# Kernel tuning notes

Measured on AMD Instinct MI355X. Metric: run time of the kernel, lower is better.

## Reference

```python
import jax, jax.numpy as jnp
import numpy as np

F_FILT = 40      # num_filters
K_GABOR = 401    # n_coefficients
K_POOL = 401     # window_length
HOP = 160        # hop_length
SR = 16000
EPS_PCEN = 1e-6
EPS_IN = 1e-5    # nn.InstanceNorm1d default eps
B, T = 8, 160000


def _hz2mel(f):
    return 2595.0 * np.log10(1.0 + f / 700.0)


def _mel2hz(m):
    return 700.0 * (10.0 ** (m / 2595.0) - 1.0)


def setup_inputs() -> dict:
    key = jax.random.key(0)
    x = jax.random.normal(key, (B, 1, T), dtype=jnp.float32)
    # mel-spaced Gabor center frequencies / bandwidths (filter_init_method='mel')
    edges = _mel2hz(np.linspace(_hz2mel(60.0), _hz2mel(7800.0), F_FILT + 2))
    center = edges[1:-1]
    fwhm = np.maximum(edges[2:] - edges[:-2], 1.0)
    eta = 2.0 * np.pi * center / SR                      # rad/sample
    sigma = np.sqrt(2.0 * np.log(2.0)) / (np.pi * fwhm / SR)  # samples
    ones = jnp.ones(F_FILT, jnp.float32)
    return {
        "x": x,
        "gabor_eta": jnp.asarray(eta, jnp.float32),
        "gabor_sigma": jnp.asarray(sigma, jnp.float32),
        "pool_bandwidths": 0.4 * ones,   # GaussianLowPass init
        "pool_bias": ones,               # GaussianLowPass bias init (ones)
        "ema_weights": 0.04 * ones,      # sPCEN smoothing_coefficient, per-channel
        "alpha": 0.96 * ones,
        "delta": 2.0 * ones,
        "root": 0.96 * ones,             # root=compression_factor=0.96
    }


def _conv1d(x, w, stride=1, groups=1):
    # x: (N, C, T), w: (O, C//groups, K); cross-correlation like torch F.conv1d
    return jax.lax.conv_general_dilated(
        x, w, (stride,), "VALID",
        dimension_numbers=("NCH", "OIH", "NCH"),
        feature_group_count=groups)


def _ema_scan(x, s):
    # y_0 = x_0 ; y_t = s*x_t + (1-s)*y_{t-1}  (per-channel s), parallel scan
    s3 = s[None, :, None]
    a = jnp.broadcast_to(1.0 - s3, x.shape)
    b = s3 * x
    a = a.at[:, :, 0].set(0.0)
    b = b.at[:, :, 0].set(x[:, :, 0])
    def comb(c1, c2):
        a1, b1 = c1
        a2, b2 = c2
        return a1 * a2, a2 * b1 + b2
    _, y = jax.lax.associative_scan(comb, (a, b), axis=2)
    return y


def reference(x, gabor_eta, gabor_sigma, pool_bandwidths, pool_bias,
              ema_weights, alpha, delta, root):
    dt = x.dtype
    # --- Gabor complex conv frontend -> |.|^2 ---
    t = jnp.arange(K_GABOR, dtype=dt) - (K_GABOR - 1) / 2.0
    env = jnp.exp(-0.5 * (t[None] / gabor_sigma[:, None]) ** 2) \
          / (jnp.sqrt(2.0 * jnp.pi) * gabor_sigma[:, None])
    phase = gabor_eta[:, None] * t[None]
    kern = jnp.stack([env * jnp.cos(phase), env * jnp.sin(phase)], axis=1)
    kern = kern.reshape(2 * F_FILT, 1, K_GABOR)
    xp = jnp.pad(x, ((0, 0), (0, 0), (K_GABOR - 1, 0)))  # causal pad
    y = _conv1d(xp, kern)                                 # (B, 2F, T)
    y = y.reshape(y.shape[0], F_FILT, 2, y.shape[-1])
    power = y[:, :, 0] ** 2 + y[:, :, 1] ** 2             # |z|^2, (B, F, T)

    # --- sPCEN compression ---
    s = jnp.clip(ema_weights, 0.0, 1.0)
    ema = _ema_scan(power, s)
    a3 = jnp.minimum(alpha, 1.0)[None, :, None]
    inv_r = (1.0 / jnp.maximum(root, 1.0))[None, :, None]
    d3 = delta[None, :, None]
    comp = (power / (EPS_PCEN + ema) ** a3 + d3) ** inv_r - d3 ** inv_r

    # --- Gaussian low-pass depthwise pooling (causal, stride=HOP) ---
    bw = jnp.clip(pool_bandwidths, 2.0 / K_POOL, 0.5)
    tp = jnp.arange(-K_POOL // 2, K_POOL // 2, dtype=dt)  # -201..199, len 401
    den = bw * 0.5 * (K_POOL - 1)
    pk = jnp.exp(-0.5 * (tp[None] / den[:, None]) ** 2).reshape(F_FILT, 1, K_POOL)
    cp = jnp.pad(comp, ((0, 0), (0, 0), (K_POOL - 1, 0)))
    pooled = _conv1d(cp, pk, stride=HOP, groups=F_FILT) + pool_bias[None, :, None]

    # --- InstanceNorm1d (affine=False, biased var, eps=1e-5) ---
    m = pooled.mean(-1, keepdims=True)
    v = pooled.var(-1, keepdims=True)
    return (pooled - m) / jnp.sqrt(v + EPS_IN)
```

## Files before the change

kernel.cpp:

```cpp
#include <hip/hip_runtime.h>
#include <math.h>

#define F_FILT   40
#define K_GABOR  401
#define HOP      160
#define T_LEN    160000
#define B_BATCH  8
#define EPS_PCENF 1e-6f
#define EPS_INF   1e-5f

#define NG       5
#define GF       8
#define NKMAX    13
#define TC       640
#define UW       10
#define NCH1     250
#define OPOFF    544
#define XPAIRS   (OPOFF + 544)
#define NSTG     136

#define THREADS  320
#define NWAVES   5
#define RT       10
#define TILE     3200
#define TPC      10
#define CHUNKS   5
#define NPT      20
#define NPOOL_BLK 200
#define KP       208
#define HALOP    200
#define TILEP    1600
#define RINGP    1800

typedef _Float16 h2_t  __attribute__((ext_vector_type(2)));
typedef _Float16 half8 __attribute__((ext_vector_type(8)));
typedef float    f32x4 __attribute__((ext_vector_type(4)));

__device__ __forceinline__ float fdot2(h2_t a, h2_t b, float c) {
    return __builtin_amdgcn_fdot2(a, b, c, false);
}
__device__ __forceinline__ unsigned pk2(float a, float b) {
    return __builtin_bit_cast(unsigned, __builtin_amdgcn_cvt_pkrtz(a, b));
}
__device__ __forceinline__ h2_t bch(unsigned u) {
    return __builtin_bit_cast(h2_t, u);
}
__device__ __forceinline__ float fexp2(float x) { return __builtin_amdgcn_exp2f(x); }
__device__ __forceinline__ float flog2(float x) { return __builtin_amdgcn_logf(x); }

__device__ __forceinline__ void group_span(float sigma0, int& klo, int& nk) {
    const int R = min(200, (int)ceilf(4.5f * sigma0));
    klo = (200 - R) & ~31;
    nk  = ((200 + R - klo) >> 5) + 1;
    if (nk > NKMAX) nk = NKMAX;
}

__global__ __launch_bounds__(256) void leaf_weights(
    const float* __restrict__ eta_g, const float* __restrict__ sigma_g,
    const float* __restrict__ bw_g,
    _Float16* __restrict__ Atab, unsigned* __restrict__ pktab)
{
    const int gi = blockIdx.x;
    const int f0 = gi * GF;
    int klo, nk;
    group_span(sigma_g[f0], klo, nk);

    for (int idx = threadIdx.x; idx < 52 * 16 * 8; idx += 256) {
        const int c8 = idx >> 7;
        const int m  = (idx >> 3) & 15;
        const int i  = idx & 7;
        const int f  = f0 + (m >> 1);
        const int k  = klo + c8 * 8 + i;
        float w = 0.f;
        if (k <= 400) {
            const float sg = sigma_g[f];
            const float t  = (float)(k - 200);
            const float z  = t / sg;
            const float e  = (0.3989422804014327f / sg) * expf(-0.5f * z * z);
            const float ph = eta_g[f] * t;
            w = (m & 1) ? e * sinf(ph) : e * cosf(ph);
        }
        Atab[(size_t)(gi * 52 + c8) * 128 + m * 8 + i] = (_Float16)w;
    }
    for (int idx = threadIdx.x; idx < GF * KP; idx += 256) {
        const int fl = idx / KP, i = idx % KP;
        const int f = f0 + fl;
        const float bw  = fminf(fmaxf(bw_g[f], 2.0f / 401.0f), 0.5f);
        const float den = bw * 0.5f * 400.0f;
        float pp[2];
        for (int j = 0; j < 2; ++j) {
            int k = 2 * i + j;
            float pv = 0.f;
            if (k < K_GABOR) {
                float tp = (float)(k - 201);
                float d = tp / den;
                pv = expf(-0.5f * d * d);
            }
            pp[j] = pv;
        }
        pktab[f * KP + i] = pk2(pp[0], pp[1]);
    }
}

__device__ __forceinline__ uint4 ld4(const unsigned* __restrict__ xp, int p) {
    uint4 v; v.x = xp[p]; v.y = xp[p + 1]; v.z = xp[p + 2]; v.w = xp[p + 3];
    return v;
}

template<int NK>
__device__ __forceinline__ void conv_kloop(
    const unsigned* __restrict__ xpair, const uint4* __restrict__ Ap,
    int aBase, int pB, f32x4* acc)
{
    uint4 F[UW];
#pragma unroll
    for (int u = 0; u < UW; ++u) F[u] = ld4(xpair, pB + 8 * u);
#pragma unroll
    for (int jk = 0; jk < NK; ++jk) {
        const half8 aCur = __builtin_bit_cast(half8, Ap[aBase + jk * 64]);
#pragma unroll
        for (int u = 0; u < UW; ++u) {
            acc[u] = __builtin_amdgcn_mfma_f32_16x16x32_f16(
                aCur, __builtin_bit_cast(half8, F[u]), acc[u], 0, 0, 0);
        }
        if (jk + 1 < NK) {
#pragma unroll
            for (int u = 0; u < UW - 2; ++u) F[u] = F[u + 2];
            F[UW - 2] = ld4(xpair, pB + 16 * (jk + 1) + 8 * (UW - 2));
            F[UW - 1] = ld4(xpair, pB + 16 * (jk + 1) + 8 * (UW - 1));
        }
    }
}

__global__ __launch_bounds__(256) void leaf_conv(
    const float* __restrict__ x,
    const float* __restrict__ sigma_g,
    const _Float16* __restrict__ Atab,
    _Float16* __restrict__ Pall)
{
    __shared__ unsigned xpair[XPAIRS];

    const int gi = blockIdx.x % NG;
    const int ch = (blockIdx.x / NG) % NCH1;
    const int b  = blockIdx.x / (NG * NCH1);
    const int f0 = gi * GF;
    const int tid = threadIdx.x;
    const int lane = tid & 63;
    const int w    = tid >> 6;

    const float* __restrict__ xb = x + (size_t)b * T_LEN;
    _Float16* __restrict__ Pb = Pall + (size_t)b * F_FILT * T_LEN;

    int klo, nk;
    group_span(sigma_g[f0], klo, nk);
    const int nkp = (nk <= 4) ? 4 : (nk <= 7) ? 7 : (nk <= 10) ? 10 : 13;
    const int t0   = ch * TC;
    const int base = t0 + klo - 400;

    if (tid < NSTG) {
        float v[9];
#pragma unroll
        for (int e = 0; e < 9; ++e) {
            const int gidx = base + 8 * tid + e;
            v[e] = (gidx >= 0 && gidx < T_LEN) ? xb[gidx] : 0.f;
        }
        uint4 pe, po;
        pe.x = pk2(v[0], v[1]); pe.y = pk2(v[2], v[3]);
        pe.z = pk2(v[4], v[5]); pe.w = pk2(v[6], v[7]);
        po.x = pk2(v[1], v[2]); po.y = pk2(v[3], v[4]);
        po.z = pk2(v[5], v[6]); po.w = pk2(v[7], v[8]);
        *(uint4*)&xpair[4 * tid]         = pe;
        *(uint4*)&xpair[OPOFF + 4 * tid] = po;
    }
    __syncthreads();

    const int n  = lane & 15;
    const int kb = lane >> 4;
    const int q0 = ((n + 8 * kb) >> 1) + ((n & 1) ? OPOFF : 0);
    const int pB = q0 + 80 * w;

    f32x4 acc[UW];
#pragma unroll
    for (int u = 0; u < UW; ++u) acc[u] = (f32x4){0.f, 0.f, 0.f, 0.f};

    const uint4* Ap = (const uint4*)Atab;
    const int aBase = (gi * 52 + kb) * 16 + n;

    switch (nkp) {
        case 4:  conv_kloop<4>(xpair, Ap, aBase, pB, acc); break;
        case 7:  conv_kloop<7>(xpair, Ap, aBase, pB, acc); break;
        case 10: conv_kloop<10>(xpair, Ap, aBase, pB, acc); break;
        default: conv_kloop<13>(xpair, Ap, aBase, pB, acc); break;
    }

    const int g  = lane >> 4;
    const int fA = f0 + 2 * g;
#pragma unroll
    for (int u = 0; u < UW; ++u) {
        const int t = t0 + (w * UW + u) * 16 + n;
        const float P0 = acc[u].x * acc[u].x + acc[u].y * acc[u].y;
        const float P1 = acc[u].z * acc[u].z + acc[u].w * acc[u].w;
        Pb[(size_t)fA * T_LEN + t]       = (_Float16)P0;
        Pb[(size_t)(fA + 1) * T_LEN + t] = (_Float16)P1;
    }
}

__global__ __launch_bounds__(THREADS) void leaf_pcen(
    const _Float16* __restrict__ Pall,
    const float* __restrict__ bias_g,
    const float* __restrict__ ema_g,
    const float* __restrict__ alpha_g,
    const float* __restrict__ delta_g,
    const float* __restrict__ root_g,
    const unsigned* __restrict__ pktab,
    float* __restrict__ outp)
{
    __shared__ unsigned ringl[RINGP];
    __shared__ unsigned pkpl[KP];
    __shared__ float pooled[NPOOL_BLK];
    __shared__ float waveV[NWAVES];
    __shared__ float p0Lds;

    const int f     = blockIdx.x % F_FILT;
    const int chunk = (blockIdx.x / F_FILT) % CHUNKS;
    const int b     = blockIdx.x / (F_FILT * CHUNKS);
    const int tid  = threadIdx.x;
    const int lane = tid & 63;
    const int wave = tid >> 6;

    const float sw    = fminf(fmaxf(ema_g[f], 0.0f), 1.0f);
    const float a     = 1.0f - sw;
    const float alpha = fminf(alpha_g[f], 1.0f);
    const float inv_r = 1.0f / fmaxf(root_g[f], 1.0f);
    const float dlt   = delta_g[f];
    const float dpow  = fexp2(inv_r * flog2(dlt));
    const bool  rt1   = (inv_r == 1.0f);

    for (int i = tid; i < RINGP; i += THREADS) ringl[i] = 0u;
    for (int i = tid; i < NPOOL_BLK; i += THREADS) pooled[i] = 0.f;
    if (tid < KP) pkpl[tid] = pktab[f * KP + tid];

    const float a2 = a * a, a4 = a2 * a2, a8 = a4 * a4;
    const float A1  = a8 * a2;
    const float A2  = A1 * A1, A4 = A2 * A2, A8 = A4 * A4;
    const float A16 = A8 * A8, A32 = A16 * A16, A64 = A32 * A32;
    float Al = 1.0f;
    if (lane & 1)  Al *= A1;
    if (lane & 2)  Al *= A2;
    if (lane & 4)  Al *= A4;
    if (lane & 8)  Al *= A8;
    if (lane & 16) Al *= A16;
    if (lane & 32) Al *= A32;

    const unsigned* PU = (const unsigned*)(Pall + ((size_t)b * F_FILT + f) * T_LEN);
    const int tile0 = chunk * TPC;
    const int itStart = (chunk == 0) ? 0 : -1;
    const unsigned P0 = 5u * (unsigned)tid;
    float carry = 0.f;

    unsigned sv[5];
    {
        const int tb = (tile0 + itStart) * 1600 + tid * 5;
#pragma unroll
        for (int q = 0; q < 5; ++q) sv[q] = PU[tb + q];
    }

    for (int it = itStart; it < TPC; ++it) {
        float p[RT];
#pragma unroll
        for (int q = 0; q < 5; ++q) {
            const h2_t hh = bch(sv[q]);
            p[2 * q]     = (float)hh.x;
            p[2 * q + 1] = (float)hh.y;
        }
        {
            const int nt = tile0 + it + 1;
            const int tb = (nt < CHUNKS * TPC ? nt : 0) * 1600 + tid * 5;
#pragma unroll
            for (int q = 0; q < 5; ++q) sv[q] = PU[tb + q];
        }

        float up[RT];
        float uu = 0.f;
#pragma unroll
        for (int r = 0; r < RT; ++r) {
            uu = fmaf(a, uu, sw * p[r]);
            up[r] = uu;
        }
        if (chunk == 0 && it == 0 && tid == 0) p0Lds = p[0];

        const bool doSlide = (it != itStart);
        unsigned tr = 0u;
        if (doSlide && tid < HALOP) tr = ringl[TILEP + tid];

        float v = uu;
        {
            float tv;
            tv = __shfl_up(v, 1);  if (lane >= 1)  v = fmaf(A1,  tv, v);
            tv = __shfl_up(v, 2);  if (lane >= 2)  v = fmaf(A2,  tv, v);
            tv = __shfl_up(v, 4);  if (lane >= 4)  v = fmaf(A4,  tv, v);
            tv = __shfl_up(v, 8);  if (lane >= 8)  v = fmaf(A8,  tv, v);
            tv = __shfl_up(v, 16); if (lane >= 16) v = fmaf(A16, tv, v);
            tv = __shfl_up(v, 32); if (lane >= 32) v = fmaf(A32, tv, v);
        }
        if (lane == 63) waveV[wave] = v;
        __syncthreads();

        if (doSlide && tid < HALOP) ringl[tid] = tr;

        float cw, cc = (chunk == 0 && it == 0) ? p0Lds : carry;
#pragma unroll
        for (int ww = 0; ww < NWAVES; ++ww) {
            if (ww == wave) cw = cc;
            cc = fmaf(A64, cc, waveV[ww]);
        }
        carry = cc;
        float cin;
        {
            float ve = __shfl_up(v, 1);
            if (lane == 0) ve = 0.f;
            cin = fmaf(Al, cw, ve);
        }

        float apr = a;
#pragma unroll
        for (int j = 0; j < 5; ++j) {
            const float e0 = fmaf(apr, cin, up[2 * j]);     apr *= a;
            const float e1 = fmaf(apr, cin, up[2 * j + 1]); apr *= a;
            const float d0 = fexp2(-alpha * flog2(EPS_PCENF + e0));
            const float d1 = fexp2(-alpha * flog2(EPS_PCENF + e1));
            float c0, c1;
            if (rt1) {
                c0 = p[2 * j] * d0;
                c1 = p[2 * j + 1] * d1;
            } else {
                const float q0 = fmaf(p[2 * j],     d0, dlt);
                const float q1 = fmaf(p[2 * j + 1], d1, dlt);
                c0 = fexp2(inv_r * flog2(q0)) - dpow;
                c1 = fexp2(inv_r * flog2(q1)) - dpow;
            }
            ringl[HALOP + P0 + j] = pk2(c0, c1);
        }
        __syncthreads();

        if (it >= 0) {
            const int o = tid >> 4, l = tid & 15;
            float part = 0.f;
#pragma unroll
            for (int t = 0; t < 13; ++t) {
                const int kpp = l + 16 * t;
                part = fdot2(bch(ringl[o * 80 + kpp]), bch(pkpl[kpp]), part);
            }
            part += __shfl_xor(part, 1, 16);
            part += __shfl_xor(part, 2, 16);
            part += __shfl_xor(part, 4, 16);
            part += __shfl_xor(part, 8, 16);
            if (l == 0) pooled[it * NPT + o] += part;
        }
    }
    __syncthreads();

    const float bias = bias_g[f];
    for (int i = tid; i < NPOOL_BLK; i += THREADS)
        outp[((size_t)b * F_FILT + f) * 1000 + (size_t)(tile0 * NPT) + i] = pooled[i] + bias;
}

__global__ __launch_bounds__(256) void leaf_norm(float* __restrict__ out)
{
    const int bf = blockIdx.x;
    float* p = out + (size_t)bf * 1000;
    __shared__ float buf[1000];
    __shared__ float red[4];
    const int tid = threadIdx.x;
    const int lane = tid & 63, wave = tid >> 6;

    float sum = 0.0f;
    for (int i = tid; i < 1000; i += 256) { float v = p[i]; buf[i] = v; sum += v; }
    for (int m = 1; m < 64; m <<= 1) sum += __shfl_xor(sum, m);
    if (lane == 0) red[wave] = sum;
    __syncthreads();
    const float mean = (red[0] + red[1] + red[2] + red[3]) * 0.001f;

    float vs = 0.0f;
    for (int i = tid; i < 1000; i += 256) { float d = buf[i] - mean; vs += d * d; }
    for (int m = 1; m < 64; m <<= 1) vs += __shfl_xor(vs, m);
    __syncthreads();
    if (lane == 0) red[wave] = vs;
    __syncthreads();
    const float var   = (red[0] + red[1] + red[2] + red[3]) * 0.001f;
    const float scale = rsqrtf(var + EPS_INF);
    for (int i = tid; i < 1000; i += 256) p[i] = (buf[i] - mean) * scale;
}

extern "C" void kernel_launch(void* const* d_in, const int* in_sizes, int n_in,
                              void* d_out, int out_size, void* d_ws, size_t ws_size,
                              hipStream_t stream)
{
    const float* x     = (const float*)d_in[0];
    const float* eta   = (const float*)d_in[1];
    const float* sigma = (const float*)d_in[2];
    const float* bw    = (const float*)d_in[3];
    const float* bias  = (const float*)d_in[4];
    const float* emaw  = (const float*)d_in[5];
    const float* alpha = (const float*)d_in[6];
    const float* delta = (const float*)d_in[7];
    const float* root  = (const float*)d_in[8];
    float* outp = (float*)d_out;

    _Float16* Atab  = (_Float16*)d_ws;
    unsigned* pktab = (unsigned*)((char*)d_ws + 133120);
    _Float16* Pall  = (_Float16*)((char*)d_ws + 166400);

    hipLaunchKernelGGL(leaf_weights, dim3(NG), dim3(256), 0, stream,
                       eta, sigma, bw, Atab, pktab);
    hipLaunchKernelGGL(leaf_conv, dim3(B_BATCH * NG * NCH1), dim3(256), 0, stream,
                       x, sigma, Atab, Pall);
    hipLaunchKernelGGL(leaf_pcen, dim3(B_BATCH * F_FILT * CHUNKS), dim3(THREADS), 0, stream,
                       Pall, bias, emaw, alpha, delta, root, pktab, outp);
    hipLaunchKernelGGL(leaf_norm, dim3(B_BATCH * F_FILT), dim3(256), 0, stream, outp);
}
```

Before: 125.0 us.

## Interleave shared x-pair layout, rotate fragment registers, add finer K-step instantiations

The shared-memory staging of half-precision sample pairs changes from separate even/odd arrays to one interleaved stream of overlapping pairs, so each lane reads strided words from a single array. The MFMA loop stops shifting its fragment registers each step and instead indexes them modulo the window, refilling two slots per K-step. More template instantiations (3, 4, 5, 7, 9, 13 K-steps) cut the padded MFMA work for filter groups with short Gabor spans. The strided LDS reads could hit different bank-conflict patterns than the old layout.

```diff
diff --git a/kernel.cpp b/kernel.cpp
--- a/kernel.cpp
+++ b/kernel.cpp
@@ -15,8 +15,7 @@
 #define TC       640
 #define UW       10
 #define NCH1     250
-#define OPOFF    544
-#define XPAIRS   (OPOFF + 544)
+#define XQW      1088
 #define NSTG     136
 
 #define THREADS  320
@@ -102,32 +101,30 @@
     }
 }
 
-__device__ __forceinline__ uint4 ld4(const unsigned* __restrict__ xp, int p) {
-    uint4 v; v.x = xp[p]; v.y = xp[p + 1]; v.z = xp[p + 2]; v.w = xp[p + 3];
+__device__ __forceinline__ uint4 ld4s(const unsigned* __restrict__ xq, int W) {
+    uint4 v; v.x = xq[W]; v.y = xq[W + 2]; v.z = xq[W + 4]; v.w = xq[W + 6];
     return v;
 }
 
 template<int NK>
 __device__ __forceinline__ void conv_kloop(
-    const unsigned* __restrict__ xpair, const uint4* __restrict__ Ap,
-    int aBase, int pB, f32x4* acc)
+    const unsigned* __restrict__ xq, const uint4* __restrict__ Ap,
+    int aBase, int wB, f32x4* acc)
 {
     uint4 F[UW];
 #pragma unroll
-    for (int u = 0; u < UW; ++u) F[u] = ld4(xpair, pB + 8 * u);
+    for (int u = 0; u < UW; ++u) F[u] = ld4s(xq, wB + 16 * u);
 #pragma unroll
     for (int jk = 0; jk < NK; ++jk) {
         const half8 aCur = __builtin_bit_cast(half8, Ap[aBase + jk * 64]);
 #pragma unroll
         for (int u = 0; u < UW; ++u) {
             acc[u] = __builtin_amdgcn_mfma_f32_16x16x32_f16(
-                aCur, __builtin_bit_cast(half8, F[u]), acc[u], 0, 0, 0);
+                aCur, __builtin_bit_cast(half8, F[(2 * jk + u) % UW]), acc[u], 0, 0, 0);
         }
         if (jk + 1 < NK) {
-#pragma unroll
-            for (int u = 0; u < UW - 2; ++u) F[u] = F[u + 2];
-            F[UW - 2] = ld4(xpair, pB + 16 * (jk + 1) + 8 * (UW - 2));
-            F[UW - 1] = ld4(xpair, pB + 16 * (jk + 1) + 8 * (UW - 1));
+            F[(2 * jk) % UW]     = ld4s(xq, wB + 32 * (jk + 1) + 16 * 8);
+            F[(2 * jk + 1) % UW] = ld4s(xq, wB + 32 * (jk + 1) + 16 * 9);
         }
     }
 }
@@ -138,7 +135,7 @@
     const _Float16* __restrict__ Atab,
     _Float16* __restrict__ Pall)
 {
-    __shared__ unsigned xpair[XPAIRS];
+    __shared__ unsigned xq[XQW];
 
     const int gi = blockIdx.x % NG;
     const int ch = (blockIdx.x / NG) % NCH1;
@@ -153,7 +150,6 @@
 
     int klo, nk;
     group_span(sigma_g[f0], klo, nk);
-    const int nkp = (nk <= 4) ? 4 : (nk <= 7) ? 7 : (nk <= 10) ? 10 : 13;
     const int t0   = ch * TC;
     const int base = t0 + klo - 400;
 
@@ -164,20 +160,19 @@
             const int gidx = base + 8 * tid + e;
             v[e] = (gidx >= 0 && gidx < T_LEN) ? xb[gidx] : 0.f;
         }
-        uint4 pe, po;
-        pe.x = pk2(v[0], v[1]); pe.y = pk2(v[2], v[3]);
-        pe.z = pk2(v[4], v[5]); pe.w = pk2(v[6], v[7]);
-        po.x = pk2(v[1], v[2]); po.y = pk2(v[3], v[4]);
-        po.z = pk2(v[5], v[6]); po.w = pk2(v[7], v[8]);
-        *(uint4*)&xpair[4 * tid]         = pe;
-        *(uint4*)&xpair[OPOFF + 4 * tid] = po;
+        uint4 w1, w2;
+        w1.x = pk2(v[0], v[1]); w1.y = pk2(v[1], v[2]);
+        w1.z = pk2(v[2], v[3]); w1.w = pk2(v[3], v[4]);
+        w2.x = pk2(v[4], v[5]); w2.y = pk2(v[5], v[6]);
+        w2.z = pk2(v[6], v[7]); w2.w = pk2(v[7], v[8]);
+        *(uint4*)&xq[8 * tid]     = w1;
+        *(uint4*)&xq[8 * tid + 4] = w2;
     }
     __syncthreads();
 
     const int n  = lane & 15;
     const int kb = lane >> 4;
-    const int q0 = ((n + 8 * kb) >> 1) + ((n & 1) ? OPOFF : 0);
-    const int pB = q0 + 80 * w;
+    const int wB = n + 8 * kb + 160 * w;
 
     f32x4 acc[UW];
 #pragma unroll
@@ -186,11 +181,15 @@
     const uint4* Ap = (const uint4*)Atab;
     const int aBase = (gi * 52 + kb) * 16 + n;
 
-    switch (nkp) {
-        case 4:  conv_kloop<4>(xpair, Ap, aBase, pB, acc); break;
-        case 7:  conv_kloop<7>(xpair, Ap, aBase, pB, acc); break;
-        case 10: conv_kloop<10>(xpair, Ap, aBase, pB, acc); break;
-        default: conv_kloop<13>(xpair, Ap, aBase, pB, acc); break;
+    switch (nk) {
+        case 3:  conv_kloop<3>(xq, Ap, aBase, wB, acc); break;
+        case 4:  conv_kloop<4>(xq, Ap, aBase, wB, acc); break;
+        case 5:  conv_kloop<5>(xq, Ap, aBase, wB, acc); break;
+        case 6:
+        case 7:  conv_kloop<7>(xq, Ap, aBase, wB, acc); break;
+        case 8:
+        case 9:  conv_kloop<9>(xq, Ap, aBase, wB, acc); break;
+        default: conv_kloop<13>(xq, Ap, aBase, wB, acc); break;
     }
 
     const int g  = lane >> 4;
```

Result: no change. 125.8 us (+0.6%).
